# Kernel tuning notes

Hardware: AMD Instinct MI355X
Metric: run time of the kernel (lower is better)

The kernel has to match this reference:

```python
import jax, jax.numpy as jnp
import numpy as np

T, B, H, L, A = 512, 128, 256, 2, 18


def setup_inputs() -> dict:
    key = jax.random.key(0)
    ks = jax.random.split(key, 10)
    s = 1.0 / np.sqrt(H)  # pytorch LSTM/Linear init scale
    return {
        "x": jax.random.normal(ks[0], (T, B, H), jnp.float32),
        "done": jax.random.bernoulli(ks[1], 0.05, (T, B)),
        "h0": jnp.zeros((L, B, H), jnp.float32),
        "c0": jnp.zeros((L, B, H), jnp.float32),
        "w_ih": jax.random.uniform(ks[2], (L, 4 * H, H), jnp.float32, -s, s),
        "w_hh": jax.random.uniform(ks[3], (L, 4 * H, H), jnp.float32, -s, s),
        "b_ih": jax.random.uniform(ks[4], (L, 4 * H), jnp.float32, -s, s),
        "b_hh": jax.random.uniform(ks[5], (L, 4 * H), jnp.float32, -s, s),
        "Wp": jax.random.uniform(ks[6], (A, H), jnp.float32, -s, s),
        "bp": jax.random.uniform(ks[7], (A,), jnp.float32, -s, s),
        "Wb": jax.random.uniform(ks[8], (1, H), jnp.float32, -s, s),
        "bb": jax.random.uniform(ks[9], (1,), jnp.float32, -s, s),
    }


def reference(x, done, h0, c0, w_ih, w_hh, b_ih, b_hh, Wp, bp, Wb, bb):
    def step(carry, inp):
        h, c = carry                      # [L,B,H] each
        xt, dt = inp                      # [B,H], [B]
        nd = (~dt).astype(xt.dtype)[None, :, None]  # reset state where done
        h = h * nd
        c = c * nd
        layer_in = xt
        hs, cs = [], []
        for l in range(L):
            gates = (layer_in @ w_ih[l].T + b_ih[l]
                     + h[l] @ w_hh[l].T + b_hh[l])      # [B,4H]
            i, f, g, o = jnp.split(gates, 4, axis=-1)   # pytorch gate order i,f,g,o
            i = jax.nn.sigmoid(i)
            f = jax.nn.sigmoid(f)
            g = jnp.tanh(g)
            o = jax.nn.sigmoid(o)
            cl = f * c[l] + i * g
            hl = o * jnp.tanh(cl)
            hs.append(hl)
            cs.append(cl)
            layer_in = hl
        return (jnp.stack(hs), jnp.stack(cs)), layer_in

    (hT, cT), core_out = jax.lax.scan(step, (h0, c0), (x, done))  # core_out: [T,B,H]
    flat = core_out.reshape(T * B, H)
    logits = flat @ Wp.T + bp                 # [T*B, A]
    baseline = (flat @ Wb.T + bb).reshape(T, B)
    action = jnp.argmax(logits, axis=1).reshape(T, B)  # eval-mode action
    policy_logits = logits.reshape(T, B, A)
    return policy_logits, baseline, action, hT, cT
```

## Files before the change

kernel.cpp:

```cpp
#include <hip/hip_runtime.h>
#include <math.h>

#define T_  512
#define B_  128
#define H_  256
#define A_  18
#define G4H 1024
#define TB_ (T_*B_)

#define OUT_BASE  (TB_*A_)
#define OUT_ACT   (OUT_BASE + TB_)
#define OUT_HT    (OUT_ACT + TB_)
#define OUT_CT    (OUT_HT + 2*B_*H_)

#define WS_H0 0
#define WS_H1 (2*B_*H_)
#define WS_C0 (4*B_*H_)
#define WS_C1 (5*B_*H_)


__global__ __launch_bounds__(512, 2) void lstm_step(
    const float* __restrict__ x, const int* __restrict__ done,
    const float* __restrict__ h0in, const float* __restrict__ c0in,
    const float* __restrict__ w_ih, const float* __restrict__ w_hh,
    const float* __restrict__ b_ih, const float* __restrict__ b_hh,
    const float* __restrict__ Wp, const float* __restrict__ bp,
    const float* __restrict__ Wb, const float* __restrict__ bb,
    float* __restrict__ out, float* __restrict__ ws, int d)
{
    __shared__ __align__(16) float gates[4][16][17];
    __shared__ float hlog[19];

    const int wg   = blockIdx.x;
    const int tid  = threadIdx.x;
    const int l    = wg >> 7;
    const int wl   = wg & 127;
    const int t    = d - l;
    const int lane = tid & 63;
    const int w    = tid >> 6;
    const int kc   = lane & 15;
    const int jq   = lane >> 4;
    const bool work   = (t >= 0 && t < T_);
    const bool dohead = (l == 1 && d >= 2);

    const int bt = wl >> 4, hg = wl & 15, b0 = bt * 16;

    if (dohead) {
        const int th = d - 2;
        const int b  = wl;
        const float* h1p = ws + WS_H1 + (size_t)(th & 1)*B_*H_ + (size_t)b*H_;
        float4 h4 = ((const float4*)h1p)[lane];
        for (int a = w; a < 19; a += 8) {
            const float* wr = (a < 18) ? (Wp + (size_t)a*H_) : Wb;
            float4 w4 = ((const float4*)wr)[lane];
            float s = w4.x*h4.x + w4.y*h4.y + w4.z*h4.z + w4.w*h4.w;
            s += __shfl_xor(s, 1);  s += __shfl_xor(s, 2);  s += __shfl_xor(s, 4);
            s += __shfl_xor(s, 8);  s += __shfl_xor(s, 16); s += __shfl_xor(s, 32);
            if (lane == 0) {
                float v = s + ((a < 18) ? bp[a] : bb[0]);
                hlog[a] = v;
                if (a < 18) out[((size_t)th*B_ + b)*A_ + a] = v;
                else        out[OUT_BASE + th*B_ + b] = v;
            }
        }
    }

    if (work) {
        const float* WI = w_ih + (size_t)l*G4H*H_;
        const float* WH = w_hh + (size_t)l*G4H*H_;
        const float* hrec = (t == 0) ? (h0in + (size_t)l*B_*H_)
                                     : (ws + (l ? WS_H1 : WS_H0) + (size_t)((t-1)&1)*B_*H_);
        const float* xin  = l ? (ws + WS_H0 + (size_t)(t&1)*B_*H_)
                              : (x + (size_t)t*B_*H_);

        float4 xr[4][4], hr[4][4];
        #pragma unroll
        for (int jj = 0; jj < 4; ++jj) {
            const int b = b0 + jq*4 + jj;
            const float nd = done[t*B_ + b] ? 0.f : 1.f;
            const float4* xb = (const float4*)(xin  + (size_t)b*H_);
            const float4* hb = (const float4*)(hrec + (size_t)b*H_);
            #pragma unroll
            for (int q = 0; q < 4; ++q) {
                xr[jj][q] = xb[q*16 + kc];
                float4 h4 = hb[q*16 + kc];
                hr[jj][q] = make_float4(h4.x*nd, h4.y*nd, h4.z*nd, h4.w*nd);
            }
        }

        #pragma unroll 2
        for (int rr = 0; rr < 8; ++rr) {
            const int wr = w*8 + rr;
            const int g  = wr >> 4, ri = wr & 15;
            const int r  = g*256 + hg*16 + ri;
            const float4* wi = (const float4*)(WI + (size_t)r*H_);
            const float4* wh = (const float4*)(WH + (size_t)r*H_);
            float4 wiv[4], whv[4];
            #pragma unroll
            for (int q = 0; q < 4; ++q) { wiv[q] = wi[q*16 + kc]; whv[q] = wh[q*16 + kc]; }
            float acc0 = 0.f, acc1 = 0.f, acc2 = 0.f, acc3 = 0.f;
            #pragma unroll
            for (int q = 0; q < 4; ++q) {
                acc0 += wiv[q].x*xr[0][q].x + wiv[q].y*xr[0][q].y + wiv[q].z*xr[0][q].z + wiv[q].w*xr[0][q].w
                      + whv[q].x*hr[0][q].x + whv[q].y*hr[0][q].y + whv[q].z*hr[0][q].z + whv[q].w*hr[0][q].w;
                acc1 += wiv[q].x*xr[1][q].x + wiv[q].y*xr[1][q].y + wiv[q].z*xr[1][q].z + wiv[q].w*xr[1][q].w
                      + whv[q].x*hr[1][q].x + whv[q].y*hr[1][q].y + whv[q].z*hr[1][q].z + whv[q].w*hr[1][q].w;
                acc2 += wiv[q].x*xr[2][q].x + wiv[q].y*xr[2][q].y + wiv[q].z*xr[2][q].z + wiv[q].w*xr[2][q].w
                      + whv[q].x*hr[2][q].x + whv[q].y*hr[2][q].y + whv[q].z*hr[2][q].z + whv[q].w*hr[2][q].w;
                acc3 += wiv[q].x*xr[3][q].x + wiv[q].y*xr[3][q].y + wiv[q].z*xr[3][q].z + wiv[q].w*xr[3][q].w
                      + whv[q].x*hr[3][q].x + whv[q].y*hr[3][q].y + whv[q].z*hr[3][q].z + whv[q].w*hr[3][q].w;
            }
            acc0 += __shfl_xor(acc0, 1, 16); acc0 += __shfl_xor(acc0, 2, 16);
            acc0 += __shfl_xor(acc0, 4, 16); acc0 += __shfl_xor(acc0, 8, 16);
            acc1 += __shfl_xor(acc1, 1, 16); acc1 += __shfl_xor(acc1, 2, 16);
            acc1 += __shfl_xor(acc1, 4, 16); acc1 += __shfl_xor(acc1, 8, 16);
            acc2 += __shfl_xor(acc2, 1, 16); acc2 += __shfl_xor(acc2, 2, 16);
            acc2 += __shfl_xor(acc2, 4, 16); acc2 += __shfl_xor(acc2, 8, 16);
            acc3 += __shfl_xor(acc3, 1, 16); acc3 += __shfl_xor(acc3, 2, 16);
            acc3 += __shfl_xor(acc3, 4, 16); acc3 += __shfl_xor(acc3, 8, 16);
            float v = (kc == 0) ? acc0 : (kc == 1) ? acc1 : (kc == 2) ? acc2 : acc3;
            if (kc < 4)
                gates[g][ri][jq*4 + kc] = v + b_ih[(size_t)l*G4H + r] + b_hh[(size_t)l*G4H + r];
        }
    }

    __syncthreads();

    if (work && tid < 256) {
        const int j = tid >> 4, hi = tid & 15;
        const int b = b0 + j, h = hg*16 + hi;
        const float nd = done[t*B_ + b] ? 0.f : 1.f;
        float* cst = ws + (l ? WS_C1 : WS_C0) + (size_t)b*H_ + h;
        float cp = ((t == 0) ? c0in[(size_t)l*B_*H_ + b*H_ + h] : *cst) * nd;
        const float gi = gates[0][hi][j], gf = gates[1][hi][j];
        const float gv = gates[2][hi][j], go = gates[3][hi][j];
        const float ii = 1.f/(1.f + expf(-gi));
        const float ff = 1.f/(1.f + expf(-gf));
        const float gt = tanhf(gv);
        const float oo = 1.f/(1.f + expf(-go));
        const float cl = ff*cp + ii*gt;
        *cst = cl;
        float* hout = ws + (l ? WS_H1 : WS_H0) + (size_t)(t&1)*B_*H_;
        hout[(size_t)b*H_ + h] = oo*tanhf(cl);
    }

    if (dohead && tid == 0) {
        const int th = d - 2;
        float best = hlog[0]; int bi = 0;
        #pragma unroll
        for (int a = 1; a < A_; ++a) { float v = hlog[a]; if (v > best) { best = v; bi = a; } }
        out[OUT_ACT + th*B_ + wl] = (float)bi;
    }

    if (l == 1 && d == 513 && tid < 256) {
        const int idx = wl*H_ + tid;
        out[OUT_HT + idx]         = ws[WS_H0 + B_*H_ + idx];
        out[OUT_HT + B_*H_ + idx] = ws[WS_H1 + B_*H_ + idx];
        out[OUT_CT + idx]         = ws[WS_C0 + idx];
        out[OUT_CT + B_*H_ + idx] = ws[WS_C1 + idx];
    }
}

extern "C" void kernel_launch(void* const* d_in, const int* in_sizes, int n_in,
                              void* d_out, int out_size, void* d_ws, size_t ws_size,
                              hipStream_t stream)
{
    const float* x    = (const float*)d_in[0];
    const int*   done = (const int*)  d_in[1];
    const float* h0   = (const float*)d_in[2];
    const float* c0   = (const float*)d_in[3];
    const float* w_ih = (const float*)d_in[4];
    const float* w_hh = (const float*)d_in[5];
    const float* b_ih = (const float*)d_in[6];
    const float* b_hh = (const float*)d_in[7];
    const float* Wp   = (const float*)d_in[8];
    const float* bp   = (const float*)d_in[9];
    const float* Wb   = (const float*)d_in[10];
    const float* bb   = (const float*)d_in[11];
    float* out = (float*)d_out;
    float* ws  = (float*)d_ws;

    for (int d = 0; d < 514; ++d) {
        lstm_step<<<dim3(256), dim3(512), 0, stream>>>(
            x, done, h0, c0, w_ih, w_hh, b_ih, b_hh, Wp, bp, Wb, bb, out, ws, d);
    }
}
```

Before: 6.792 ms.

## Batch eight wavefront steps per launch with grid barriers and LDS-resident weights

```diff
diff --git a/kernel.cpp b/kernel.cpp
--- a/kernel.cpp
+++ b/kernel.cpp
@@ -13,21 +13,26 @@
 #define OUT_HT    (OUT_ACT + TB_)
 #define OUT_CT    (OUT_HT + 2*B_*H_)
 
-#define WS_H0 0
-#define WS_H1 (2*B_*H_)
-#define WS_C0 (4*B_*H_)
-#define WS_C1 (5*B_*H_)
-
-
-__global__ __launch_bounds__(512, 2) void lstm_step(
+#define WS_H0  0
+#define WS_H1  (2*B_*H_)
+#define WS_C0  (4*B_*H_)
+#define WS_C1  (5*B_*H_)
+#define WS_CTR (6*B_*H_)
+
+#define S_    8
+#define NDISP 65
+
+
+__global__ __launch_bounds__(512, 1) void lstm_multi(
     const float* __restrict__ x, const int* __restrict__ done,
     const float* __restrict__ h0in, const float* __restrict__ c0in,
     const float* __restrict__ w_ih, const float* __restrict__ w_hh,
     const float* __restrict__ b_ih, const float* __restrict__ b_hh,
     const float* __restrict__ Wp, const float* __restrict__ bp,
     const float* __restrict__ Wb, const float* __restrict__ bb,
-    float* __restrict__ out, float* __restrict__ ws, int d)
+    float* __restrict__ out, float* __restrict__ ws, int dsp)
 {
+    __shared__ __align__(16) float wlds[64*2*H_];
     __shared__ __align__(16) float gates[4][16][17];
     __shared__ float hlog[19];
 
@@ -35,129 +40,190 @@
     const int tid  = threadIdx.x;
     const int l    = wg >> 7;
     const int wl   = wg & 127;
-    const int t    = d - l;
     const int lane = tid & 63;
     const int w    = tid >> 6;
     const int kc   = lane & 15;
     const int jq   = lane >> 4;
-    const bool work   = (t >= 0 && t < T_);
-    const bool dohead = (l == 1 && d >= 2);
-
-    const int bt = wl >> 4, hg = wl & 15, b0 = bt * 16;
-
-    if (dohead) {
-        const int th = d - 2;
-        const int b  = wl;
-        const float* h1p = ws + WS_H1 + (size_t)(th & 1)*B_*H_ + (size_t)b*H_;
-        float4 h4 = ((const float4*)h1p)[lane];
-        for (int a = w; a < 19; a += 8) {
-            const float* wr = (a < 18) ? (Wp + (size_t)a*H_) : Wb;
-            float4 w4 = ((const float4*)wr)[lane];
-            float s = w4.x*h4.x + w4.y*h4.y + w4.z*h4.z + w4.w*h4.w;
-            s += __shfl_xor(s, 1);  s += __shfl_xor(s, 2);  s += __shfl_xor(s, 4);
-            s += __shfl_xor(s, 8);  s += __shfl_xor(s, 16); s += __shfl_xor(s, 32);
-            if (lane == 0) {
-                float v = s + ((a < 18) ? bp[a] : bb[0]);
-                hlog[a] = v;
-                if (a < 18) out[((size_t)th*B_ + b)*A_ + a] = v;
-                else        out[OUT_BASE + th*B_ + b] = v;
-            }
-        }
-    }
-
-    if (work) {
+    const int bt   = wl >> 4, hg = wl & 15, b0 = bt*16;
+
+    {
         const float* WI = w_ih + (size_t)l*G4H*H_;
         const float* WH = w_hh + (size_t)l*G4H*H_;
-        const float* hrec = (t == 0) ? (h0in + (size_t)l*B_*H_)
-                                     : (ws + (l ? WS_H1 : WS_H0) + (size_t)((t-1)&1)*B_*H_);
-        const float* xin  = l ? (ws + WS_H0 + (size_t)(t&1)*B_*H_)
-                              : (x + (size_t)t*B_*H_);
-
-        float4 xr[4][4], hr[4][4];
+        float4* dst = (float4*)wlds;
         #pragma unroll
-        for (int jj = 0; jj < 4; ++jj) {
-            const int b = b0 + jq*4 + jj;
+        for (int k = 0; k < 16; ++k) {
+            const int idx = k*512 + tid;
+            const int rs = idx >> 7, rem = idx & 127;
+            const int m = rem >> 6, q4 = rem & 63;
+            const int r = (rs >> 4)*256 + hg*16 + (rs & 15);
+            const float* src = (m ? WH : WI) + (size_t)r*H_;
+            dst[idx] = ((const float4*)src)[q4];
+        }
+    }
+
+    float bsum[8];
+    #pragma unroll
+    for (int rr = 0; rr < 8; ++rr) {
+        const int rs = w*8 + rr;
+        const int r  = (rs >> 4)*256 + hg*16 + (rs & 15);
+        bsum[rr] = b_ih[(size_t)l*G4H + r] + b_hh[(size_t)l*G4H + r];
+    }
+    float4 wpr[3]; float wpb[3];
+    if (l == 1) {
+        #pragma unroll
+        for (int k = 0; k < 3; ++k) {
+            const int a = w + 8*k;
+            if (a < 19) {
+                const float* wr = (a < 18) ? (Wp + (size_t)a*H_) : Wb;
+                wpr[k] = ((const float4*)wr)[lane];
+                wpb[k] = (a < 18) ? bp[a] : bb[0];
+            }
+        }
+    }
+    float cr = 0.f; bool chave = false;
+
+    unsigned int* ctr = (unsigned int*)(ws + WS_CTR);
+    __syncthreads();
+
+    for (int p = 0; p < S_; ++p) {
+        const int d = dsp*S_ + p;
+        const int t = d - l;
+        const bool work   = (t >= 0 && t < T_);
+        const bool dohead = (l == 1 && d >= 2 && d - 2 < T_);
+
+        if (dohead) {
+            const int th = d - 2;
+            const float* h1p = ws + WS_H1 + (size_t)(th & 1)*B_*H_ + (size_t)wl*H_;
+            float4 h4 = ((const float4*)h1p)[lane];
+            #pragma unroll
+            for (int k = 0; k < 3; ++k) {
+                const int a = w + 8*k;
+                if (a < 19) {
+                    float s = wpr[k].x*h4.x + wpr[k].y*h4.y + wpr[k].z*h4.z + wpr[k].w*h4.w;
+                    s += __shfl_xor(s, 1);  s += __shfl_xor(s, 2);  s += __shfl_xor(s, 4);
+                    s += __shfl_xor(s, 8);  s += __shfl_xor(s, 16); s += __shfl_xor(s, 32);
+                    if (lane == 0) {
+                        float v = s + wpb[k];
+                        hlog[a] = v;
+                        if (a < 18) out[((size_t)th*B_ + wl)*A_ + a] = v;
+                        else        out[OUT_BASE + th*B_ + wl] = v;
+                    }
+                }
+            }
+        }
+
+        if (work) {
+            const float* hrec = (t == 0) ? (h0in + (size_t)l*B_*H_)
+                                         : (ws + (l ? WS_H1 : WS_H0) + (size_t)((t-1)&1)*B_*H_);
+            const float* xin  = l ? (ws + WS_H0 + (size_t)(t&1)*B_*H_)
+                                  : (x + (size_t)t*B_*H_);
+            float4 xr[4][4], hr[4][4];
+            #pragma unroll
+            for (int jj = 0; jj < 4; ++jj) {
+                const int b = b0 + jq*4 + jj;
+                const float nd = done[t*B_ + b] ? 0.f : 1.f;
+                const float4* xb = (const float4*)(xin  + (size_t)b*H_);
+                const float4* hb = (const float4*)(hrec + (size_t)b*H_);
+                #pragma unroll
+                for (int q = 0; q < 4; ++q) {
+                    xr[jj][q] = xb[q*16 + kc];
+                    float4 h4 = hb[q*16 + kc];
+                    hr[jj][q] = make_float4(h4.x*nd, h4.y*nd, h4.z*nd, h4.w*nd);
+                }
+            }
+            const float4* wl4 = (const float4*)wlds;
+            #pragma unroll 2
+            for (int rr = 0; rr < 8; ++rr) {
+                const int rs = w*8 + rr;
+                const int g  = rs >> 4, ri = rs & 15;
+                const int wb4 = rs*128;
+                float4 wiv[4], whv[4];
+                #pragma unroll
+                for (int q = 0; q < 4; ++q) {
+                    wiv[q] = wl4[wb4 + q*16 + kc];
+                    whv[q] = wl4[wb4 + 64 + q*16 + kc];
+                }
+                float acc0 = 0.f, acc1 = 0.f, acc2 = 0.f, acc3 = 0.f;
+                #pragma unroll
+                for (int q = 0; q < 4; ++q) {
+                    acc0 += wiv[q].x*xr[0][q].x + wiv[q].y*xr[0][q].y + wiv[q].z*xr[0][q].z + wiv[q].w*xr[0][q].w
+                          + whv[q].x*hr[0][q].x + whv[q].y*hr[0][q].y + whv[q].z*hr[0][q].z + whv[q].w*hr[0][q].w;
+                    acc1 += wiv[q].x*xr[1][q].x + wiv[q].y*xr[1][q].y + wiv[q].z*xr[1][q].z + wiv[q].w*xr[1][q].w
+                          + whv[q].x*hr[1][q].x + whv[q].y*hr[1][q].y + whv[q].z*hr[1][q].z + whv[q].w*hr[1][q].w;
+                    acc2 += wiv[q].x*xr[2][q].x + wiv[q].y*xr[2][q].y + wiv[q].z*xr[2][q].z + wiv[q].w*xr[2][q].w
+                          + whv[q].x*hr[2][q].x + whv[q].y*hr[2][q].y + whv[q].z*hr[2][q].z + whv[q].w*hr[2][q].w;
+                    acc3 += wiv[q].x*xr[3][q].x + wiv[q].y*xr[3][q].y + wiv[q].z*xr[3][q].z + wiv[q].w*xr[3][q].w
+                          + whv[q].x*hr[3][q].x + whv[q].y*hr[3][q].y + whv[q].z*hr[3][q].z + whv[q].w*hr[3][q].w;
+                }
+                acc0 += __shfl_xor(acc0, 1, 16); acc0 += __shfl_xor(acc0, 2, 16);
+                acc0 += __shfl_xor(acc0, 4, 16); acc0 += __shfl_xor(acc0, 8, 16);
+                acc1 += __shfl_xor(acc1, 1, 16); acc1 += __shfl_xor(acc1, 2, 16);
+                acc1 += __shfl_xor(acc1, 4, 16); acc1 += __shfl_xor(acc1, 8, 16);
+                acc2 += __shfl_xor(acc2, 1, 16); acc2 += __shfl_xor(acc2, 2, 16);
+                acc2 += __shfl_xor(acc2, 4, 16); acc2 += __shfl_xor(acc2, 8, 16);
+                acc3 += __shfl_xor(acc3, 1, 16); acc3 += __shfl_xor(acc3, 2, 16);
+                acc3 += __shfl_xor(acc3, 4, 16); acc3 += __shfl_xor(acc3, 8, 16);
+                float v = (kc == 0) ? acc0 : (kc == 1) ? acc1 : (kc == 2) ? acc2 : acc3;
+                if (kc < 4)
+                    gates[g][ri][jq*4 + kc] = v + bsum[rr];
+            }
+        }
+
+        __syncthreads();
+
+        if (work && tid < 256) {
+            const int j = tid >> 4, hi = tid & 15;
+            const int b = b0 + j, h = hg*16 + hi;
             const float nd = done[t*B_ + b] ? 0.f : 1.f;
-            const float4* xb = (const float4*)(xin  + (size_t)b*H_);
-            const float4* hb = (const float4*)(hrec + (size_t)b*H_);
+            float* cst = ws + (l ? WS_C1 : WS_C0) + (size_t)b*H_ + h;
+            if (!chave) {
+                cr = (t == 0) ? c0in[(size_t)l*B_*H_ + b*H_ + h] : *cst;
+                chave = true;
+            }
+            float cp = cr * nd;
+            const float gi = gates[0][hi][j], gf = gates[1][hi][j];
+            const float gv = gates[2][hi][j], go = gates[3][hi][j];
+            const float ii = 1.f/(1.f + expf(-gi));
+            const float ff = 1.f/(1.f + expf(-gf));
+            const float gt = tanhf(gv);
+            const float oo = 1.f/(1.f + expf(-go));
+            const float cl = ff*cp + ii*gt;
+            cr = cl;
+            *cst = cl;
+            float* hout = ws + (l ? WS_H1 : WS_H0) + (size_t)(t&1)*B_*H_;
+            hout[(size_t)b*H_ + h] = oo*tanhf(cl);
+        }
+
+        if (dohead && tid == 0) {
+            const int th = d - 2;
+            float best = hlog[0]; int bi = 0;
             #pragma unroll
-            for (int q = 0; q < 4; ++q) {
-                xr[jj][q] = xb[q*16 + kc];
-                float4 h4 = hb[q*16 + kc];
-                hr[jj][q] = make_float4(h4.x*nd, h4.y*nd, h4.z*nd, h4.w*nd);
-            }
-        }
-
-        #pragma unroll 2
-        for (int rr = 0; rr < 8; ++rr) {
-            const int wr = w*8 + rr;
-            const int g  = wr >> 4, ri = wr & 15;
-            const int r  = g*256 + hg*16 + ri;
-            const float4* wi = (const float4*)(WI + (size_t)r*H_);
-            const float4* wh = (const float4*)(WH + (size_t)r*H_);
-            float4 wiv[4], whv[4];
-            #pragma unroll
-            for (int q = 0; q < 4; ++q) { wiv[q] = wi[q*16 + kc]; whv[q] = wh[q*16 + kc]; }
-            float acc0 = 0.f, acc1 = 0.f, acc2 = 0.f, acc3 = 0.f;
-            #pragma unroll
-            for (int q = 0; q < 4; ++q) {
-                acc0 += wiv[q].x*xr[0][q].x + wiv[q].y*xr[0][q].y + wiv[q].z*xr[0][q].z + wiv[q].w*xr[0][q].w
-                      + whv[q].x*hr[0][q].x + whv[q].y*hr[0][q].y + whv[q].z*hr[0][q].z + whv[q].w*hr[0][q].w;
-                acc1 += wiv[q].x*xr[1][q].x + wiv[q].y*xr[1][q].y + wiv[q].z*xr[1][q].z + wiv[q].w*xr[1][q].w
-                      + whv[q].x*hr[1][q].x + whv[q].y*hr[1][q].y + whv[q].z*hr[1][q].z + whv[q].w*hr[1][q].w;
-                acc2 += wiv[q].x*xr[2][q].x + wiv[q].y*xr[2][q].y + wiv[q].z*xr[2][q].z + wiv[q].w*xr[2][q].w
-                      + whv[q].x*hr[2][q].x + whv[q].y*hr[2][q].y + whv[q].z*hr[2][q].z + whv[q].w*hr[2][q].w;
-                acc3 += wiv[q].x*xr[3][q].x + wiv[q].y*xr[3][q].y + wiv[q].z*xr[3][q].z + wiv[q].w*xr[3][q].w
-                      + whv[q].x*hr[3][q].x + whv[q].y*hr[3][q].y + whv[q].z*hr[3][q].z + whv[q].w*hr[3][q].w;
-            }
-            acc0 += __shfl_xor(acc0, 1, 16); acc0 += __shfl_xor(acc0, 2, 16);
-            acc0 += __shfl_xor(acc0, 4, 16); acc0 += __shfl_xor(acc0, 8, 16);
-            acc1 += __shfl_xor(acc1, 1, 16); acc1 += __shfl_xor(acc1, 2, 16);
-            acc1 += __shfl_xor(acc1, 4, 16); acc1 += __shfl_xor(acc1, 8, 16);
-            acc2 += __shfl_xor(acc2, 1, 16); acc2 += __shfl_xor(acc2, 2, 16);
-            acc2 += __shfl_xor(acc2, 4, 16); acc2 += __shfl_xor(acc2, 8, 16);
-            acc3 += __shfl_xor(acc3, 1, 16); acc3 += __shfl_xor(acc3, 2, 16);
-            acc3 += __shfl_xor(acc3, 4, 16); acc3 += __shfl_xor(acc3, 8, 16);
-            float v = (kc == 0) ? acc0 : (kc == 1) ? acc1 : (kc == 2) ? acc2 : acc3;
-            if (kc < 4)
-                gates[g][ri][jq*4 + kc] = v + b_ih[(size_t)l*G4H + r] + b_hh[(size_t)l*G4H + r];
-        }
-    }
-
-    __syncthreads();
-
-    if (work && tid < 256) {
-        const int j = tid >> 4, hi = tid & 15;
-        const int b = b0 + j, h = hg*16 + hi;
-        const float nd = done[t*B_ + b] ? 0.f : 1.f;
-        float* cst = ws + (l ? WS_C1 : WS_C0) + (size_t)b*H_ + h;
-        float cp = ((t == 0) ? c0in[(size_t)l*B_*H_ + b*H_ + h] : *cst) * nd;
-        const float gi = gates[0][hi][j], gf = gates[1][hi][j];
-        const float gv = gates[2][hi][j], go = gates[3][hi][j];
-        const float ii = 1.f/(1.f + expf(-gi));
-        const float ff = 1.f/(1.f + expf(-gf));
-        const float gt = tanhf(gv);
-        const float oo = 1.f/(1.f + expf(-go));
-        const float cl = ff*cp + ii*gt;
-        *cst = cl;
-        float* hout = ws + (l ? WS_H1 : WS_H0) + (size_t)(t&1)*B_*H_;
-        hout[(size_t)b*H_ + h] = oo*tanhf(cl);
-    }
-
-    if (dohead && tid == 0) {
-        const int th = d - 2;
-        float best = hlog[0]; int bi = 0;
-        #pragma unroll
-        for (int a = 1; a < A_; ++a) { float v = hlog[a]; if (v > best) { best = v; bi = a; } }
-        out[OUT_ACT + th*B_ + wl] = (float)bi;
-    }
-
-    if (l == 1 && d == 513 && tid < 256) {
-        const int idx = wl*H_ + tid;
-        out[OUT_HT + idx]         = ws[WS_H0 + B_*H_ + idx];
-        out[OUT_HT + B_*H_ + idx] = ws[WS_H1 + B_*H_ + idx];
-        out[OUT_CT + idx]         = ws[WS_C0 + idx];
-        out[OUT_CT + B_*H_ + idx] = ws[WS_C1 + idx];
+            for (int a = 1; a < A_; ++a) { float v = hlog[a]; if (v > best) { best = v; bi = a; } }
+            out[OUT_ACT + th*B_ + wl] = (float)bi;
+        }
+
+        if (l == 1 && d == 513 && tid < 256) {
+            const int idx = wl*H_ + tid;
+            out[OUT_HT + idx]         = ws[WS_H0 + B_*H_ + idx];
+            out[OUT_HT + B_*H_ + idx] = ws[WS_H1 + B_*H_ + idx];
+            out[OUT_CT + idx]         = ws[WS_C0 + idx];
+            out[OUT_CT + B_*H_ + idx] = ws[WS_C1 + idx];
+        }
+
+        if (d >= 513) break;
+
+        if (p < S_ - 1) {
+            __syncthreads();
+            if (tid == 0) {
+                unsigned int* cell = ctr + (dsp*(S_-1) + p);
+                __builtin_amdgcn_fence(__ATOMIC_RELEASE, "agent");
+                __hip_atomic_fetch_add(cell, 1u, __ATOMIC_RELAXED, __HIP_MEMORY_SCOPE_AGENT);
+                while (__hip_atomic_load(cell, __ATOMIC_RELAXED, __HIP_MEMORY_SCOPE_AGENT) < 256u)
+                    __builtin_amdgcn_s_sleep(2);
+                __builtin_amdgcn_fence(__ATOMIC_ACQUIRE, "agent");
+            }
+            __syncthreads();
+        }
     }
 }
 
@@ -180,8 +246,10 @@
     float* out = (float*)d_out;
     float* ws  = (float*)d_ws;
 
-    for (int d = 0; d < 514; ++d) {
-        lstm_step<<<dim3(256), dim3(512), 0, stream>>>(
-            x, done, h0, c0, w_ih, w_hh, b_ih, b_hh, Wp, bp, Wb, bb, out, ws, d);
+    hipMemsetAsync((char*)d_ws + (size_t)WS_CTR*sizeof(float), 0, 2048, stream);
+
+    for (int dsp = 0; dsp < NDISP; ++dsp) {
+        lstm_multi<<<dim3(256), dim3(512), 0, stream>>>(
+            x, done, h0, c0, w_ih, w_hh, b_ih, b_hh, Wp, bp, Wb, bb, out, ws, dsp);
     }
 }
```

Result: slower. 11.10 ms (+63.4%).
